# Optimization experiments

Measured on AMD Instinct MI355X. Metric: run time of the kernel, lower is better.

## Reference

```python
import jax, jax.numpy as jnp
import numpy as np

TWO_PI = 2.0 * np.pi
LN_EPS = 1e-5


def _gelu(x):
    return jax.nn.gelu(x, approximate=False)


def _layer_norm(h):
    mu = jnp.mean(h, axis=-1, keepdims=True)
    var = jnp.mean(jnp.square(h - mu), axis=-1, keepdims=True)
    return (h - mu) * jax.lax.rsqrt(var + LN_EPS)


def _torsion_field(x, W, b, tf, tc):
    # x: [B, in], W: [out, in], tf: [order, out, in], tc: scalar
    base = x @ W.T + b
    corr = jnp.zeros_like(base)
    order = tf.shape[0]
    for n in range(order):
        lo = x @ tf[n].T  # [B, out]
        phase = TWO_PI * (n + 1) * lo / (jnp.mean(jnp.abs(lo)) + 1e-8)
        corr = corr + jnp.sin(phase) * lo / (n + 1)
    return base + jax.nn.sigmoid(tc) * corr


def setup_inputs() -> dict:
    key = jax.random.key(0)
    ks = jax.random.split(key, 16)
    B, D_IN, D_R, D_I, D_O, D_H = 2097152, 6, 4, 16, 4, 8
    ts = 0.1
    inp = {
        "x": jax.random.normal(ks[0], (B, D_IN), dtype=jnp.float32),
        # input_projection
        "W_in": jax.random.normal(ks[1], (D_R, D_IN), dtype=jnp.float32) * 0.1,
        "b_in": jnp.zeros((D_R,), jnp.float32),
        # layer1_reciprocal (MiniTorsionField, order=2)
        "r_w": jax.random.normal(ks[2], (D_R, D_R), dtype=jnp.float32) * 0.1,
        "r_b": jnp.zeros((D_R,), jnp.float32),
        "r_tf": jax.random.normal(ks[3], (2, D_R, D_R), dtype=jnp.float32) * ts,
        "r_tc": jnp.float32(0.5),
        # layer1_internal (MiniTorsionField, order=3, strength*0.8)
        "i_w": jax.random.normal(ks[4], (D_I, D_I), dtype=jnp.float32) * 0.1,
        "i_b": jnp.zeros((D_I,), jnp.float32),
        "i_tf": jax.random.normal(ks[5], (3, D_I, D_I), dtype=jnp.float32) * (ts * 0.8),
        "i_tc": jnp.float32(0.5),
        # cross flows
        "W_ri": jax.random.normal(ks[6], (D_I, D_R), dtype=jnp.float32) * 0.1,
        "b_ri": jnp.zeros((D_I,), jnp.float32),
        "W_ir": jax.random.normal(ks[7], (D_R, D_I), dtype=jnp.float32) * 0.1,
        "b_ir": jnp.zeros((D_R,), jnp.float32),
        "flow_gate": jnp.float32(0.5),
        "mem": jax.random.normal(ks[8], (1, D_I), dtype=jnp.float32) * 0.01,
        # output projection: Linear(4,8) -> GELU -> Linear(8,4)
        "W_o1": jax.random.normal(ks[9], (D_H, D_R), dtype=jnp.float32) * 0.1,
        "b_o1": jnp.zeros((D_H,), jnp.float32),
        "W_o2": jax.random.normal(ks[10], (D_O, D_H), dtype=jnp.float32) * 0.1,
        "b_o2": jnp.zeros((D_O,), jnp.float32),
    }
    return inp


def reference(x, W_in, b_in, r_w, r_b, r_tf, r_tc, i_w, i_b, i_tf, i_tc,
              W_ri, b_ri, W_ir, b_ir, flow_gate, mem, W_o1, b_o1, W_o2, b_o2):
    B = x.shape[0]
    x_recip = _gelu(x @ W_in.T + b_in)                      # [B, 4]
    x_internal = jnp.broadcast_to(mem, (B, mem.shape[1]))   # [B, 16]

    h_r = _gelu(_layer_norm(_torsion_field(x_recip, r_w, r_b, r_tf, r_tc)))
    h_i = _gelu(_layer_norm(_torsion_field(x_internal, i_w, i_b, i_tf, i_tc)))

    gate = jax.nn.sigmoid(flow_gate)
    h_i = h_i + gate * (h_r @ W_ri.T + b_ri)
    h_r = h_r + gate * (h_i @ W_ir.T + b_ir)

    out = _gelu(h_r @ W_o1.T + b_o1) @ W_o2.T + b_o2        # [B, 4]
    return out
```

## Files before the change

kernel.cpp:

```cpp
#include <hip/hip_runtime.h>
#include <math.h>

#define TWO_PI_F 6.2831853071795864769f

__device__ __forceinline__ float gelu_f(float v) {
    const float y  = v * 0.70710678118654752f;
    const float ay = fabsf(y);
    const float t  = __builtin_amdgcn_rcpf(fmaf(0.3275911f, ay, 1.0f));
    const float e  = __builtin_amdgcn_exp2f(-1.4426950408889634f * y * y);
    float p = fmaf(1.061405429f, t, -1.453152027f);
    p = fmaf(p, t, 1.421413741f);
    p = fmaf(p, t, -0.284496736f);
    p = fmaf(p, t, 0.254829592f);
    const float erf_abs = 1.0f - p * t * e;
    const float erf_v   = copysignf(erf_abs, v);
    const float hv = 0.5f * v;
    return fmaf(hv, erf_v, hv);
}

__global__ __launch_bounds__(256) void k_sum(
    const float* __restrict__ x,
    const float* __restrict__ W_in, const float* __restrict__ b_in,
    const float* __restrict__ r_tf, const float* __restrict__ r_tc,
    const float* __restrict__ i_w,  const float* __restrict__ i_b,
    const float* __restrict__ i_tf, const float* __restrict__ i_tc,
    const float* __restrict__ W_ri, const float* __restrict__ b_ri,
    const float* __restrict__ W_ir, const float* __restrict__ b_ir,
    const float* __restrict__ flow_gate, const float* __restrict__ mem,
    float2* __restrict__ partials, float* __restrict__ cst, int B)
{
    const int tid = threadIdx.x;
    __shared__ float s_hc[16];
    __shared__ float s_red[8];

    if (blockIdx.x == 0 && tid < 64) {
        const int j = tid & 15;
        float base = i_b[j];
#pragma unroll
        for (int k = 0; k < 16; ++k) base = fmaf(i_w[j*16 + k], mem[k], base);
        float corr = 0.f;
#pragma unroll
        for (int n = 0; n < 3; ++n) {
            float lo = 0.f;
#pragma unroll
            for (int k = 0; k < 16; ++k) lo = fmaf(i_tf[n*256 + j*16 + k], mem[k], lo);
            float a = fabsf(lo);
            a += __shfl_xor(a, 1); a += __shfl_xor(a, 2); a += __shfl_xor(a, 4); a += __shfl_xor(a, 8);
            const float mean = a * (1.0f/16.0f);
            const float phase = TWO_PI_F * (float)(n+1) * lo / (mean + 1e-8f);
            corr = fmaf(sinf(phase), lo / (float)(n+1), corr);
        }
        const float sc = 1.0f / (1.0f + expf(-i_tc[0]));
        const float t = fmaf(sc, corr, base);
        float mu = t;
        mu += __shfl_xor(mu, 1); mu += __shfl_xor(mu, 2); mu += __shfl_xor(mu, 4); mu += __shfl_xor(mu, 8);
        mu *= (1.0f/16.0f);
        const float d = t - mu;
        float v = d*d;
        v += __shfl_xor(v, 1); v += __shfl_xor(v, 2); v += __shfl_xor(v, 4); v += __shfl_xor(v, 8);
        v *= (1.0f/16.0f);
        const float h = gelu_f(d * rsqrtf(v + 1e-5f));
        if (tid < 16) s_hc[j] = h;
    }
    __syncthreads();
    if (blockIdx.x == 0) {
        const float g = 1.0f / (1.0f + expf(-flow_gate[0]));
        if (tid < 4) {
            float acc = 0.f;
#pragma unroll
            for (int m = 0; m < 16; ++m) acc = fmaf(W_ir[tid*16 + m], fmaf(g, b_ri[m], s_hc[m]), acc);
            cst[24 + tid] = g * (acc + b_ir[tid]);
        }
        if (tid < 16) {
            const int l = tid >> 2, j = tid & 3;
            float M = 0.f;
#pragma unroll
            for (int m = 0; m < 16; ++m) M = fmaf(W_ir[l*16 + m], W_ri[m*4 + j], M);
            cst[8 + tid] = g * g * M;
        }
        if (tid == 0) cst[2] = 1.0f / (1.0f + expf(-r_tc[0]));
    }

    const int npairs = B >> 1;
    const int TT = gridDim.x * blockDim.x;
    const int gtid = blockIdx.x * blockDim.x + tid;
    float s0 = 0.f, s1 = 0.f;
    for (int p = gtid; p < npairs; p += TT) {
        const float4* xp = (const float4*)(x + (size_t)p * 12);
        float4 q0 = xp[0], q1 = xp[1], q2 = xp[2];
        float xv[2][6] = {{q0.x, q0.y, q0.z, q0.w, q1.x, q1.y},
                          {q1.z, q1.w, q2.x, q2.y, q2.z, q2.w}};
#pragma unroll
        for (int r = 0; r < 2; ++r) {
            float xr[4];
#pragma unroll
            for (int j = 0; j < 4; ++j) {
                float a = b_in[j];
#pragma unroll
                for (int k = 0; k < 6; ++k) a = fmaf(W_in[j*6+k], xv[r][k], a);
                xr[j] = gelu_f(a);
            }
#pragma unroll
            for (int j = 0; j < 4; ++j) {
                float l0 = 0.f, l1 = 0.f;
#pragma unroll
                for (int k = 0; k < 4; ++k) {
                    l0 = fmaf(r_tf[j*4+k],      xr[k], l0);
                    l1 = fmaf(r_tf[16 + j*4+k], xr[k], l1);
                }
                s0 += fabsf(l0);
                s1 += fabsf(l1);
            }
        }
    }
    if ((B & 1) && gtid == 0) {
        const float* xs = x + (size_t)(B-1) * 6;
        float xr[4];
#pragma unroll
        for (int j = 0; j < 4; ++j) {
            float a = b_in[j];
#pragma unroll
            for (int k = 0; k < 6; ++k) a = fmaf(W_in[j*6+k], xs[k], a);
            xr[j] = gelu_f(a);
        }
#pragma unroll
        for (int j = 0; j < 4; ++j) {
            float l0 = 0.f, l1 = 0.f;
#pragma unroll
            for (int k = 0; k < 4; ++k) {
                l0 = fmaf(r_tf[j*4+k],      xr[k], l0);
                l1 = fmaf(r_tf[16 + j*4+k], xr[k], l1);
            }
            s0 += fabsf(l0);
            s1 += fabsf(l1);
        }
    }
#pragma unroll
    for (int off = 32; off > 0; off >>= 1) {
        s0 += __shfl_down(s0, off);
        s1 += __shfl_down(s1, off);
    }
    if ((tid & 63) == 0) { s_red[(tid>>6)*2] = s0; s_red[(tid>>6)*2+1] = s1; }
    __syncthreads();
    if (tid == 0) {
        partials[blockIdx.x] = make_float2(s_red[0]+s_red[2]+s_red[4]+s_red[6],
                                           s_red[1]+s_red[3]+s_red[5]+s_red[7]);
    }
}

__global__ __launch_bounds__(256) void k_main(
    const float* __restrict__ x,
    const float* __restrict__ W_in, const float* __restrict__ b_in,
    const float* __restrict__ r_w,  const float* __restrict__ r_b,
    const float* __restrict__ r_tf,
    const float* __restrict__ W_o1, const float* __restrict__ b_o1,
    const float* __restrict__ W_o2, const float* __restrict__ b_o2,
    const float2* __restrict__ partials, int nb,
    const float* __restrict__ cst,
    float* __restrict__ out, int B)
{
    const int tid = threadIdx.x;
    __shared__ float s_red[8];
    __shared__ float s_c[2];

    float t0 = 0.f, t1 = 0.f;
    for (int k = tid; k < nb; k += 256) {
        const float2 pr = partials[k];
        t0 += pr.x; t1 += pr.y;
    }
#pragma unroll
    for (int off = 32; off > 0; off >>= 1) {
        t0 += __shfl_down(t0, off);
        t1 += __shfl_down(t1, off);
    }
    if ((tid & 63) == 0) { s_red[(tid>>6)*2] = t0; s_red[(tid>>6)*2+1] = t1; }
    __syncthreads();
    if (tid == 0) {
        const float u0 = s_red[0]+s_red[2]+s_red[4]+s_red[6];
        const float u1 = s_red[1]+s_red[3]+s_red[5]+s_red[7];
        const float m0 = u0 / (4.0f * (float)B);
        const float m1 = u1 / (4.0f * (float)B);
        s_c[0] = TWO_PI_F * 1.0f / (m0 + 1e-8f);
        s_c[1] = TWO_PI_F * 2.0f / (m1 + 1e-8f);
    }
    __syncthreads();
    const float c0 = s_c[0], c1 = s_c[1];
    const float sr = cst[2];

    float m4[16], cvec[4];
#pragma unroll
    for (int i = 0; i < 16; ++i) m4[i] = cst[8 + i];
#pragma unroll
    for (int i = 0; i < 4; ++i)  cvec[i] = cst[24 + i];

    const int npairs = B >> 1;
    const int TT = gridDim.x * blockDim.x;
    const int gtid = blockIdx.x * blockDim.x + tid;

    for (int p = gtid; p < npairs; p += TT) {
        const float4* xp = (const float4*)(x + (size_t)p * 12);
        float4 q0 = xp[0], q1 = xp[1], q2 = xp[2];
        float xv[2][6] = {{q0.x, q0.y, q0.z, q0.w, q1.x, q1.y},
                          {q1.z, q1.w, q2.x, q2.y, q2.z, q2.w}};
#pragma unroll
        for (int r = 0; r < 2; ++r) {
            float xr[4];
#pragma unroll
            for (int j = 0; j < 4; ++j) {
                float a = b_in[j];
#pragma unroll
                for (int k = 0; k < 6; ++k) a = fmaf(W_in[j*6+k], xv[r][k], a);
                xr[j] = gelu_f(a);
            }
            float t[4];
#pragma unroll
            for (int j = 0; j < 4; ++j) {
                float l0 = 0.f, l1 = 0.f, bse = r_b[j];
#pragma unroll
                for (int k = 0; k < 4; ++k) {
                    l0  = fmaf(r_tf[j*4+k],      xr[k], l0);
                    l1  = fmaf(r_tf[16 + j*4+k], xr[k], l1);
                    bse = fmaf(r_w[j*4+k],       xr[k], bse);
                }
                const float corr = __sinf(c0 * l0) * l0 + 0.5f * __sinf(c1 * l1) * l1;
                t[j] = fmaf(sr, corr, bse);
            }
            const float mu = 0.25f * (t[0] + t[1] + t[2] + t[3]);
            float d0 = t[0]-mu, d1 = t[1]-mu, d2 = t[2]-mu, d3 = t[3]-mu;
            const float var = 0.25f * (d0*d0 + d1*d1 + d2*d2 + d3*d3);
            const float inv = rsqrtf(var + 1e-5f);
            float hr[4] = { gelu_f(d0*inv), gelu_f(d1*inv), gelu_f(d2*inv), gelu_f(d3*inv) };

            float h2[4];
#pragma unroll
            for (int l = 0; l < 4; ++l) {
                float a = hr[l] + cvec[l];
#pragma unroll
                for (int j = 0; j < 4; ++j) a = fmaf(m4[l*4+j], hr[j], a);
                h2[l] = a;
            }
            float hid[8];
#pragma unroll
            for (int h = 0; h < 8; ++h) {
                float a = b_o1[h];
#pragma unroll
                for (int l = 0; l < 4; ++l) a = fmaf(W_o1[h*4+l], h2[l], a);
                hid[h] = gelu_f(a);
            }
            float o[4];
#pragma unroll
            for (int oo = 0; oo < 4; ++oo) {
                float a = b_o2[oo];
#pragma unroll
                for (int h = 0; h < 8; ++h) a = fmaf(W_o2[oo*8+h], hid[h], a);
                o[oo] = a;
            }
            ((float4*)out)[(size_t)2*p + r] = make_float4(o[0], o[1], o[2], o[3]);
        }
    }

    if ((B & 1) && gtid == 0) {
        const float* xs = x + (size_t)(B-1) * 6;
        float xr[4];
#pragma unroll
        for (int j = 0; j < 4; ++j) {
            float a = b_in[j];
#pragma unroll
            for (int k = 0; k < 6; ++k) a = fmaf(W_in[j*6+k], xs[k], a);
            xr[j] = gelu_f(a);
        }
        float t[4];
#pragma unroll
        for (int j = 0; j < 4; ++j) {
            float l0 = 0.f, l1 = 0.f, bse = r_b[j];
#pragma unroll
            for (int k = 0; k < 4; ++k) {
                l0  = fmaf(r_tf[j*4+k],      xr[k], l0);
                l1  = fmaf(r_tf[16 + j*4+k], xr[k], l1);
                bse = fmaf(r_w[j*4+k],       xr[k], bse);
            }
            const float corr = __sinf(c0 * l0) * l0 + 0.5f * __sinf(c1 * l1) * l1;
            t[j] = fmaf(sr, corr, bse);
        }
        const float mu = 0.25f * (t[0] + t[1] + t[2] + t[3]);
        float d0 = t[0]-mu, d1 = t[1]-mu, d2 = t[2]-mu, d3 = t[3]-mu;
        const float var = 0.25f * (d0*d0 + d1*d1 + d2*d2 + d3*d3);
        const float inv = rsqrtf(var + 1e-5f);
        float hr[4] = { gelu_f(d0*inv), gelu_f(d1*inv), gelu_f(d2*inv), gelu_f(d3*inv) };
        float h2[4];
#pragma unroll
        for (int l = 0; l < 4; ++l) {
            float a = hr[l] + cvec[l];
#pragma unroll
            for (int j = 0; j < 4; ++j) a = fmaf(m4[l*4+j], hr[j], a);
            h2[l] = a;
        }
        float hid[8];
#pragma unroll
        for (int h = 0; h < 8; ++h) {
            float a = b_o1[h];
#pragma unroll
            for (int l = 0; l < 4; ++l) a = fmaf(W_o1[h*4+l], h2[l], a);
            hid[h] = gelu_f(a);
        }
        float o[4];
#pragma unroll
        for (int oo = 0; oo < 4; ++oo) {
            float a = b_o2[oo];
#pragma unroll
            for (int h = 0; h < 8; ++h) a = fmaf(W_o2[oo*8+h], hid[h], a);
            o[oo] = a;
        }
        ((float4*)out)[(size_t)B - 1] = make_float4(o[0], o[1], o[2], o[3]);
    }
}

extern "C" void kernel_launch(void* const* d_in, const int* in_sizes, int n_in,
                              void* d_out, int out_size, void* d_ws, size_t ws_size,
                              hipStream_t stream)
{
    const float* x    = (const float*)d_in[0];
    const float* W_in = (const float*)d_in[1];
    const float* b_in = (const float*)d_in[2];
    const float* r_w  = (const float*)d_in[3];
    const float* r_b  = (const float*)d_in[4];
    const float* r_tf = (const float*)d_in[5];
    const float* r_tc = (const float*)d_in[6];
    const float* i_w  = (const float*)d_in[7];
    const float* i_b  = (const float*)d_in[8];
    const float* i_tf = (const float*)d_in[9];
    const float* i_tc = (const float*)d_in[10];
    const float* W_ri = (const float*)d_in[11];
    const float* b_ri = (const float*)d_in[12];
    const float* W_ir = (const float*)d_in[13];
    const float* b_ir = (const float*)d_in[14];
    const float* fg   = (const float*)d_in[15];
    const float* mem  = (const float*)d_in[16];
    const float* W_o1 = (const float*)d_in[17];
    const float* b_o1 = (const float*)d_in[18];
    const float* W_o2 = (const float*)d_in[19];
    const float* b_o2 = (const float*)d_in[20];
    float* out = (float*)d_out;
    float* ws  = (float*)d_ws;

    const int B = in_sizes[0] / 6;

    int NB1 = 1024;
    const long cap = (long)(ws_size / 4) - 64;
    if (cap < 2L * NB1) NB1 = (int)(cap / 2);
    if (NB1 < 1) NB1 = 1;
    float*  cst      = ws;
    float2* partials = (float2*)(ws + 64);

    k_sum<<<NB1, 256, 0, stream>>>(x, W_in, b_in, r_tf, r_tc, i_w, i_b, i_tf, i_tc,
                                   W_ri, b_ri, W_ir, b_ir, fg, mem, partials, cst, B);

    int NB2 = 2048;
    const int npairs = B >> 1;
    if (NB2 * 256 > npairs + 255) NB2 = (npairs + 255) / 256;
    if (NB2 < 1) NB2 = 1;
    k_main<<<NB2, 256, 0, stream>>>(x, W_in, b_in, r_w, r_b, r_tf,
                                    W_o1, b_o1, W_o2, b_o2,
                                    partials, NB1, cst, out, B);
}
```

Baseline: 53.05 us.

## Pack two rows into float2 math, fold constants, and use cheaper GELU and sin

Both kernels now process the two rows of each pair together using float2 vector types and element-wise FMA, which can map to packed FP32 instructions. Weights are folded ahead of time: sigmoid and 2π factors go into the torsion weights, and the cross-flow matrix and offset are merged into the first output layer, computed once in block 0. GELU uses a shorter erf polynomial, sin uses the hardware revolution-based instruction, and outputs are written with nontemporal stores. Grid size and launch bounds also change; the lower-order erf approximation adds some numerical error.

```diff
diff --git a/kernel.cpp b/kernel.cpp
--- a/kernel.cpp
+++ b/kernel.cpp
@@ -3,22 +3,58 @@
 
 #define TWO_PI_F 6.2831853071795864769f
 
-__device__ __forceinline__ float gelu_f(float v) {
+typedef float v2f __attribute__((ext_vector_type(2)));
+typedef float v4f __attribute__((ext_vector_type(4)));
+
+static __device__ __forceinline__ v2f v2s(float s) { return (v2f){s, s}; }
+
+static __device__ __forceinline__ v2f fma2(v2f a, v2f b, v2f c) {
+#if __has_builtin(__builtin_elementwise_fma)
+    return __builtin_elementwise_fma(a, b, c);
+#else
+    return (v2f){ fmaf(a.x, b.x, c.x), fmaf(a.y, b.y, c.y) };
+#endif
+}
+
+static __device__ __forceinline__ float sin_rev(float x) {
+#if __has_builtin(__builtin_amdgcn_sinf)
+    return __builtin_amdgcn_sinf(x);
+#else
+    return __sinf(TWO_PI_F * x);
+#endif
+}
+
+static __device__ __forceinline__ float gelu_s(float v) {
     const float y  = v * 0.70710678118654752f;
     const float ay = fabsf(y);
-    const float t  = __builtin_amdgcn_rcpf(fmaf(0.3275911f, ay, 1.0f));
-    const float e  = __builtin_amdgcn_exp2f(-1.4426950408889634f * y * y);
-    float p = fmaf(1.061405429f, t, -1.453152027f);
-    p = fmaf(p, t, 1.421413741f);
-    p = fmaf(p, t, -0.284496736f);
-    p = fmaf(p, t, 0.254829592f);
+    const float t  = __builtin_amdgcn_rcpf(fmaf(0.47047f, ay, 1.0f));
+    const float e  = __builtin_amdgcn_exp2f(y * y * -1.4426950408889634f);
+    float p = fmaf(0.7478556f, t, -0.0958798f);
+    p = fmaf(p, t, 0.3480242f);
     const float erf_abs = 1.0f - p * t * e;
-    const float erf_v   = copysignf(erf_abs, v);
+    const float erf_v   = __builtin_copysignf(erf_abs, v);
     const float hv = 0.5f * v;
     return fmaf(hv, erf_v, hv);
 }
 
-__global__ __launch_bounds__(256) void k_sum(
+static __device__ __forceinline__ v2f gelu2(v2f v) {
+    v2f y  = v * 0.70710678118654752f;
+    v2f ay = (v2f){ fabsf(y.x), fabsf(y.y) };
+    v2f td = fma2(v2s(0.47047f), ay, v2s(1.0f));
+    v2f t  = (v2f){ __builtin_amdgcn_rcpf(td.x), __builtin_amdgcn_rcpf(td.y) };
+    v2f yy = y * y;
+    v2f e  = (v2f){ __builtin_amdgcn_exp2f(yy.x * -1.4426950408889634f),
+                    __builtin_amdgcn_exp2f(yy.y * -1.4426950408889634f) };
+    v2f p  = fma2(v2s(0.7478556f), t, v2s(-0.0958798f));
+    p = fma2(p, t, v2s(0.3480242f));
+    v2f erfabs = v2s(1.0f) - (p * t) * e;
+    v2f erf = (v2f){ __builtin_copysignf(erfabs.x, v.x),
+                     __builtin_copysignf(erfabs.y, v.y) };
+    v2f hv = v * 0.5f;
+    return fma2(hv, erf, hv);
+}
+
+__global__ __launch_bounds__(256, 8) void k_sum(
     const float* __restrict__ x,
     const float* __restrict__ W_in, const float* __restrict__ b_in,
     const float* __restrict__ r_tf, const float* __restrict__ r_tc,
@@ -27,92 +63,112 @@
     const float* __restrict__ W_ri, const float* __restrict__ b_ri,
     const float* __restrict__ W_ir, const float* __restrict__ b_ir,
     const float* __restrict__ flow_gate, const float* __restrict__ mem,
+    const float* __restrict__ W_o1, const float* __restrict__ b_o1,
     float2* __restrict__ partials, float* __restrict__ cst, int B)
 {
     const int tid = threadIdx.x;
-    __shared__ float s_hc[16];
-    __shared__ float s_red[8];
-
-    if (blockIdx.x == 0 && tid < 64) {
-        const int j = tid & 15;
-        float base = i_b[j];
-#pragma unroll
-        for (int k = 0; k < 16; ++k) base = fmaf(i_w[j*16 + k], mem[k], base);
-        float corr = 0.f;
-#pragma unroll
-        for (int n = 0; n < 3; ++n) {
-            float lo = 0.f;
-#pragma unroll
-            for (int k = 0; k < 16; ++k) lo = fmaf(i_tf[n*256 + j*16 + k], mem[k], lo);
-            float a = fabsf(lo);
-            a += __shfl_xor(a, 1); a += __shfl_xor(a, 2); a += __shfl_xor(a, 4); a += __shfl_xor(a, 8);
-            const float mean = a * (1.0f/16.0f);
-            const float phase = TWO_PI_F * (float)(n+1) * lo / (mean + 1e-8f);
-            corr = fmaf(sinf(phase), lo / (float)(n+1), corr);
-        }
-        const float sc = 1.0f / (1.0f + expf(-i_tc[0]));
-        const float t = fmaf(sc, corr, base);
-        float mu = t;
-        mu += __shfl_xor(mu, 1); mu += __shfl_xor(mu, 2); mu += __shfl_xor(mu, 4); mu += __shfl_xor(mu, 8);
-        mu *= (1.0f/16.0f);
-        const float d = t - mu;
-        float v = d*d;
-        v += __shfl_xor(v, 1); v += __shfl_xor(v, 2); v += __shfl_xor(v, 4); v += __shfl_xor(v, 8);
-        v *= (1.0f/16.0f);
-        const float h = gelu_f(d * rsqrtf(v + 1e-5f));
-        if (tid < 16) s_hc[j] = h;
-    }
-    __syncthreads();
+    __shared__ float s_hc[16], s_cv[4], s_m4[16], s_red[8];
+
     if (blockIdx.x == 0) {
-        const float g = 1.0f / (1.0f + expf(-flow_gate[0]));
+        if (tid < 64) {
+            const int j = tid & 15;
+            float base = i_b[j];
+#pragma unroll
+            for (int k = 0; k < 16; ++k) base = fmaf(i_w[j*16 + k], mem[k], base);
+            float corr = 0.f;
+#pragma unroll
+            for (int n = 0; n < 3; ++n) {
+                float lo = 0.f;
+#pragma unroll
+                for (int k = 0; k < 16; ++k) lo = fmaf(i_tf[n*256 + j*16 + k], mem[k], lo);
+                float a = fabsf(lo);
+                a += __shfl_xor(a, 1); a += __shfl_xor(a, 2);
+                a += __shfl_xor(a, 4); a += __shfl_xor(a, 8);
+                const float mean = a * (1.0f/16.0f);
+                const float phase = TWO_PI_F * (float)(n+1) * lo / (mean + 1e-8f);
+                corr = fmaf(sinf(phase), lo / (float)(n+1), corr);
+            }
+            const float sc = 1.0f / (1.0f + expf(-i_tc[0]));
+            const float t = fmaf(sc, corr, base);
+            float mu = t;
+            mu += __shfl_xor(mu, 1); mu += __shfl_xor(mu, 2);
+            mu += __shfl_xor(mu, 4); mu += __shfl_xor(mu, 8);
+            mu *= (1.0f/16.0f);
+            const float d = t - mu;
+            float v = d*d;
+            v += __shfl_xor(v, 1); v += __shfl_xor(v, 2);
+            v += __shfl_xor(v, 4); v += __shfl_xor(v, 8);
+            v *= (1.0f/16.0f);
+            const float h = gelu_s(d * rsqrtf(v + 1e-5f));
+            if (tid < 16) s_hc[j] = h;
+        }
+        __syncthreads();
+        const float g  = 1.0f / (1.0f + expf(-flow_gate[0]));
+        const float sr = 1.0f / (1.0f + expf(-r_tc[0]));
         if (tid < 4) {
             float acc = 0.f;
 #pragma unroll
-            for (int m = 0; m < 16; ++m) acc = fmaf(W_ir[tid*16 + m], fmaf(g, b_ri[m], s_hc[m]), acc);
-            cst[24 + tid] = g * (acc + b_ir[tid]);
+            for (int m = 0; m < 16; ++m)
+                acc = fmaf(W_ir[tid*16 + m], fmaf(g, b_ri[m], s_hc[m]), acc);
+            s_cv[tid] = g * (acc + b_ir[tid]);
         }
         if (tid < 16) {
             const int l = tid >> 2, j = tid & 3;
             float M = 0.f;
 #pragma unroll
             for (int m = 0; m < 16; ++m) M = fmaf(W_ir[l*16 + m], W_ri[m*4 + j], M);
-            cst[8 + tid] = g * g * M;
-        }
-        if (tid == 0) cst[2] = 1.0f / (1.0f + expf(-r_tc[0]));
+            s_m4[tid] = g * g * M;
+            cst[8  + tid] = sr * r_tf[tid];
+            cst[24 + tid] = 0.5f * sr * r_tf[16 + tid];
+        }
+        if (tid == 0) cst[0] = sr;
+        __syncthreads();
+        if (tid < 32) {
+            const int h = tid >> 2, j = tid & 3;
+            float we = 0.f;
+#pragma unroll
+            for (int l = 0; l < 4; ++l)
+                we = fmaf(W_o1[h*4 + l], ((l == j) ? 1.0f : 0.0f) + s_m4[l*4 + j], we);
+            cst[40 + tid] = we;
+        }
+        if (tid < 8) {
+            float be = b_o1[tid];
+#pragma unroll
+            for (int l = 0; l < 4; ++l) be = fmaf(W_o1[tid*4 + l], s_cv[l], be);
+            cst[72 + tid] = be;
+        }
     }
 
     const int npairs = B >> 1;
     const int TT = gridDim.x * blockDim.x;
     const int gtid = blockIdx.x * blockDim.x + tid;
-    float s0 = 0.f, s1 = 0.f;
+    v2f a0 = v2s(0.f), a1 = v2s(0.f);
     for (int p = gtid; p < npairs; p += TT) {
         const float4* xp = (const float4*)(x + (size_t)p * 12);
         float4 q0 = xp[0], q1 = xp[1], q2 = xp[2];
-        float xv[2][6] = {{q0.x, q0.y, q0.z, q0.w, q1.x, q1.y},
-                          {q1.z, q1.w, q2.x, q2.y, q2.z, q2.w}};
-#pragma unroll
-        for (int r = 0; r < 2; ++r) {
-            float xr[4];
-#pragma unroll
-            for (int j = 0; j < 4; ++j) {
-                float a = b_in[j];
-#pragma unroll
-                for (int k = 0; k < 6; ++k) a = fmaf(W_in[j*6+k], xv[r][k], a);
-                xr[j] = gelu_f(a);
+        v2f xv[6] = { {q0.x, q1.z}, {q0.y, q1.w}, {q0.z, q2.x},
+                      {q0.w, q2.y}, {q1.x, q2.z}, {q1.y, q2.w} };
+        v2f xr[4];
+#pragma unroll
+        for (int j = 0; j < 4; ++j) {
+            v2f a = v2s(b_in[j]);
+#pragma unroll
+            for (int k = 0; k < 6; ++k) a = fma2(v2s(W_in[j*6+k]), xv[k], a);
+            xr[j] = gelu2(a);
+        }
+#pragma unroll
+        for (int j = 0; j < 4; ++j) {
+            v2f l0 = v2s(0.f), l1 = v2s(0.f);
+#pragma unroll
+            for (int k = 0; k < 4; ++k) {
+                l0 = fma2(v2s(r_tf[j*4+k]),      xr[k], l0);
+                l1 = fma2(v2s(r_tf[16 + j*4+k]), xr[k], l1);
             }
-#pragma unroll
-            for (int j = 0; j < 4; ++j) {
-                float l0 = 0.f, l1 = 0.f;
-#pragma unroll
-                for (int k = 0; k < 4; ++k) {
-                    l0 = fmaf(r_tf[j*4+k],      xr[k], l0);
-                    l1 = fmaf(r_tf[16 + j*4+k], xr[k], l1);
-                }
-                s0 += fabsf(l0);
-                s1 += fabsf(l1);
-            }
-        }
-    }
+            a0 += (v2f){ fabsf(l0.x), fabsf(l0.y) };
+            a1 += (v2f){ fabsf(l1.x), fabsf(l1.y) };
+        }
+    }
+    float s0 = a0.x + a0.y, s1 = a1.x + a1.y;
     if ((B & 1) && gtid == 0) {
         const float* xs = x + (size_t)(B-1) * 6;
         float xr[4];
@@ -121,7 +177,7 @@
             float a = b_in[j];
 #pragma unroll
             for (int k = 0; k < 6; ++k) a = fmaf(W_in[j*6+k], xs[k], a);
-            xr[j] = gelu_f(a);
+            xr[j] = gelu_s(a);
         }
 #pragma unroll
         for (int j = 0; j < 4; ++j) {
@@ -148,12 +204,10 @@
     }
 }
 
-__global__ __launch_bounds__(256) void k_main(
+__global__ __launch_bounds__(256, 4) void k_main(
     const float* __restrict__ x,
     const float* __restrict__ W_in, const float* __restrict__ b_in,
     const float* __restrict__ r_w,  const float* __restrict__ r_b,
-    const float* __restrict__ r_tf,
-    const float* __restrict__ W_o1, const float* __restrict__ b_o1,
     const float* __restrict__ W_o2, const float* __restrict__ b_o2,
     const float2* __restrict__ partials, int nb,
     const float* __restrict__ cst,
@@ -175,23 +229,17 @@
     }
     if ((tid & 63) == 0) { s_red[(tid>>6)*2] = t0; s_red[(tid>>6)*2+1] = t1; }
     __syncthreads();
+    const float sr = cst[0];
     if (tid == 0) {
         const float u0 = s_red[0]+s_red[2]+s_red[4]+s_red[6];
         const float u1 = s_red[1]+s_red[3]+s_red[5]+s_red[7];
         const float m0 = u0 / (4.0f * (float)B);
         const float m1 = u1 / (4.0f * (float)B);
-        s_c[0] = TWO_PI_F * 1.0f / (m0 + 1e-8f);
-        s_c[1] = TWO_PI_F * 2.0f / (m1 + 1e-8f);
+        s_c[0] = 1.0f / ((m0 + 1e-8f) * sr);
+        s_c[1] = 4.0f / ((m1 + 1e-8f) * sr);
     }
     __syncthreads();
-    const float c0 = s_c[0], c1 = s_c[1];
-    const float sr = cst[2];
-
-    float m4[16], cvec[4];
-#pragma unroll
-    for (int i = 0; i < 16; ++i) m4[i] = cst[8 + i];
-#pragma unroll
-    for (int i = 0; i < 4; ++i)  cvec[i] = cst[24 + i];
+    const float C0 = s_c[0], C1 = s_c[1];
 
     const int npairs = B >> 1;
     const int TT = gridDim.x * blockDim.x;
@@ -200,63 +248,63 @@
     for (int p = gtid; p < npairs; p += TT) {
         const float4* xp = (const float4*)(x + (size_t)p * 12);
         float4 q0 = xp[0], q1 = xp[1], q2 = xp[2];
-        float xv[2][6] = {{q0.x, q0.y, q0.z, q0.w, q1.x, q1.y},
-                          {q1.z, q1.w, q2.x, q2.y, q2.z, q2.w}};
-#pragma unroll
-        for (int r = 0; r < 2; ++r) {
-            float xr[4];
-#pragma unroll
-            for (int j = 0; j < 4; ++j) {
-                float a = b_in[j];
-#pragma unroll
-                for (int k = 0; k < 6; ++k) a = fmaf(W_in[j*6+k], xv[r][k], a);
-                xr[j] = gelu_f(a);
+        v2f xv[6] = { {q0.x, q1.z}, {q0.y, q1.w}, {q0.z, q2.x},
+                      {q0.w, q2.y}, {q1.x, q2.z}, {q1.y, q2.w} };
+
+        v2f xr[4];
+#pragma unroll
+        for (int j = 0; j < 4; ++j) {
+            v2f a = v2s(b_in[j]);
+#pragma unroll
+            for (int k = 0; k < 6; ++k) a = fma2(v2s(W_in[j*6+k]), xv[k], a);
+            xr[j] = gelu2(a);
+        }
+
+        v2f t[4];
+#pragma unroll
+        for (int j = 0; j < 4; ++j) {
+            v2f L0 = v2s(0.f), L1 = v2s(0.f), bse = v2s(r_b[j]);
+#pragma unroll
+            for (int k = 0; k < 4; ++k) {
+                L0  = fma2(v2s(cst[8  + j*4+k]), xr[k], L0);
+                L1  = fma2(v2s(cst[24 + j*4+k]), xr[k], L1);
+                bse = fma2(v2s(r_w[j*4+k]),      xr[k], bse);
             }
-            float t[4];
-#pragma unroll
-            for (int j = 0; j < 4; ++j) {
-                float l0 = 0.f, l1 = 0.f, bse = r_b[j];
-#pragma unroll
-                for (int k = 0; k < 4; ++k) {
-                    l0  = fmaf(r_tf[j*4+k],      xr[k], l0);
-                    l1  = fmaf(r_tf[16 + j*4+k], xr[k], l1);
-                    bse = fmaf(r_w[j*4+k],       xr[k], bse);
-                }
-                const float corr = __sinf(c0 * l0) * l0 + 0.5f * __sinf(c1 * l1) * l1;
-                t[j] = fmaf(sr, corr, bse);
-            }
-            const float mu = 0.25f * (t[0] + t[1] + t[2] + t[3]);
-            float d0 = t[0]-mu, d1 = t[1]-mu, d2 = t[2]-mu, d3 = t[3]-mu;
-            const float var = 0.25f * (d0*d0 + d1*d1 + d2*d2 + d3*d3);
-            const float inv = rsqrtf(var + 1e-5f);
-            float hr[4] = { gelu_f(d0*inv), gelu_f(d1*inv), gelu_f(d2*inv), gelu_f(d3*inv) };
-
-            float h2[4];
-#pragma unroll
-            for (int l = 0; l < 4; ++l) {
-                float a = hr[l] + cvec[l];
-#pragma unroll
-                for (int j = 0; j < 4; ++j) a = fmaf(m4[l*4+j], hr[j], a);
-                h2[l] = a;
-            }
-            float hid[8];
-#pragma unroll
-            for (int h = 0; h < 8; ++h) {
-                float a = b_o1[h];
-#pragma unroll
-                for (int l = 0; l < 4; ++l) a = fmaf(W_o1[h*4+l], h2[l], a);
-                hid[h] = gelu_f(a);
-            }
-            float o[4];
-#pragma unroll
-            for (int oo = 0; oo < 4; ++oo) {
-                float a = b_o2[oo];
-#pragma unroll
-                for (int h = 0; h < 8; ++h) a = fmaf(W_o2[oo*8+h], hid[h], a);
-                o[oo] = a;
-            }
-            ((float4*)out)[(size_t)2*p + r] = make_float4(o[0], o[1], o[2], o[3]);
-        }
+            v2f sa = (v2f){ sin_rev(C0 * L0.x), sin_rev(C0 * L0.y) };
+            v2f sb = (v2f){ sin_rev(C1 * L1.x), sin_rev(C1 * L1.y) };
+            t[j] = fma2(sa, L0, fma2(sb, L1, bse));
+        }
+
+        const v2f mu = (t[0] + t[1] + t[2] + t[3]) * 0.25f;
+        v2f d0 = t[0]-mu, d1 = t[1]-mu, d2 = t[2]-mu, d3 = t[3]-mu;
+        v2f var = d0*d0;
+        var = fma2(d1, d1, var);
+        var = fma2(d2, d2, var);
+        var = fma2(d3, d3, var);
+        var = var * 0.25f + 1e-5f;
+        const v2f inv = (v2f){ __builtin_amdgcn_rsqf(var.x), __builtin_amdgcn_rsqf(var.y) };
+        v2f hr[4] = { gelu2(d0*inv), gelu2(d1*inv), gelu2(d2*inv), gelu2(d3*inv) };
+
+        v2f hid[8];
+#pragma unroll
+        for (int h = 0; h < 8; ++h) {
+            v2f a = v2s(cst[72 + h]);
+#pragma unroll
+            for (int j = 0; j < 4; ++j) a = fma2(v2s(cst[40 + h*4+j]), hr[j], a);
+            hid[h] = gelu2(a);
+        }
+        v2f o[4];
+#pragma unroll
+        for (int oo = 0; oo < 4; ++oo) {
+            v2f a = v2s(b_o2[oo]);
+#pragma unroll
+            for (int h = 0; h < 8; ++h) a = fma2(v2s(W_o2[oo*8+h]), hid[h], a);
+            o[oo] = a;
+        }
+        v4f r0 = (v4f){ o[0].x, o[1].x, o[2].x, o[3].x };
+        v4f r1 = (v4f){ o[0].y, o[1].y, o[2].y, o[3].y };
+        __builtin_nontemporal_store(r0, (v4f*)out + (size_t)2*p);
+        __builtin_nontemporal_store(r1, (v4f*)out + (size_t)2*p + 1);
     }
 
     if ((B & 1) && gtid == 0) {
@@ -267,41 +315,32 @@
             float a = b_in[j];
 #pragma unroll
             for (int k = 0; k < 6; ++k) a = fmaf(W_in[j*6+k], xs[k], a);
-            xr[j] = gelu_f(a);
+            xr[j] = gelu_s(a);
         }
         float t[4];
 #pragma unroll
         for (int j = 0; j < 4; ++j) {
-            float l0 = 0.f, l1 = 0.f, bse = r_b[j];
+            float L0 = 0.f, L1 = 0.f, bse = r_b[j];
 #pragma unroll
             for (int k = 0; k < 4; ++k) {
-                l0  = fmaf(r_tf[j*4+k],      xr[k], l0);
-                l1  = fmaf(r_tf[16 + j*4+k], xr[k], l1);
-                bse = fmaf(r_w[j*4+k],       xr[k], bse);
+                L0  = fmaf(cst[8  + j*4+k], xr[k], L0);
+                L1  = fmaf(cst[24 + j*4+k], xr[k], L1);
+                bse = fmaf(r_w[j*4+k],      xr[k], bse);
             }
-            const float corr = __sinf(c0 * l0) * l0 + 0.5f * __sinf(c1 * l1) * l1;
-            t[j] = fmaf(sr, corr, bse);
-        }
-        const float mu = 0.25f * (t[0] + t[1] + t[2] + t[3]);
-        float d0 = t[0]-mu, d1 = t[1]-mu, d2 = t[2]-mu, d3 = t[3]-mu;
+            t[j] = fmaf(sin_rev(C0*L0), L0, fmaf(sin_rev(C1*L1), L1, bse));
+        }
+        const float mu = 0.25f * (t[0]+t[1]+t[2]+t[3]);
+        float d0=t[0]-mu, d1=t[1]-mu, d2=t[2]-mu, d3=t[3]-mu;
         const float var = 0.25f * (d0*d0 + d1*d1 + d2*d2 + d3*d3);
-        const float inv = rsqrtf(var + 1e-5f);
-        float hr[4] = { gelu_f(d0*inv), gelu_f(d1*inv), gelu_f(d2*inv), gelu_f(d3*inv) };
-        float h2[4];
-#pragma unroll
-        for (int l = 0; l < 4; ++l) {
-            float a = hr[l] + cvec[l];
-#pragma unroll
-            for (int j = 0; j < 4; ++j) a = fmaf(m4[l*4+j], hr[j], a);
-            h2[l] = a;
-        }
+        const float inv = __builtin_amdgcn_rsqf(var + 1e-5f);
+        float hr[4] = { gelu_s(d0*inv), gelu_s(d1*inv), gelu_s(d2*inv), gelu_s(d3*inv) };
         float hid[8];
 #pragma unroll
         for (int h = 0; h < 8; ++h) {
-            float a = b_o1[h];
-#pragma unroll
-            for (int l = 0; l < 4; ++l) a = fmaf(W_o1[h*4+l], h2[l], a);
-            hid[h] = gelu_f(a);
+            float a = cst[72 + h];
+#pragma unroll
+            for (int j = 0; j < 4; ++j) a = fmaf(cst[40 + h*4+j], hr[j], a);
+            hid[h] = gelu_s(a);
         }
         float o[4];
 #pragma unroll
@@ -344,22 +383,22 @@
     float* ws  = (float*)d_ws;
 
     const int B = in_sizes[0] / 6;
+    const int npairs = B >> 1;
 
     int NB1 = 1024;
-    const long cap = (long)(ws_size / 4) - 64;
+    const long cap = (long)(ws_size / 4) - 128;
     if (cap < 2L * NB1) NB1 = (int)(cap / 2);
     if (NB1 < 1) NB1 = 1;
     float*  cst      = ws;
-    float2* partials = (float2*)(ws + 64);
+    float2* partials = (float2*)(ws + 128);
 
     k_sum<<<NB1, 256, 0, stream>>>(x, W_in, b_in, r_tf, r_tc, i_w, i_b, i_tf, i_tc,
-                                   W_ri, b_ri, W_ir, b_ir, fg, mem, partials, cst, B);
-
-    int NB2 = 2048;
-    const int npairs = B >> 1;
-    if (NB2 * 256 > npairs + 255) NB2 = (npairs + 255) / 256;
+                                   W_ri, b_ri, W_ir, b_ir, fg, mem, W_o1, b_o1,
+                                   partials, cst, B);
+
+    int NB2 = (npairs + 511) / 512;
     if (NB2 < 1) NB2 = 1;
-    k_main<<<NB2, 256, 0, stream>>>(x, W_in, b_in, r_w, r_b, r_tf,
-                                    W_o1, b_o1, W_o2, b_o2,
+    if (NB2 > 8192) NB2 = 8192;
+    k_main<<<NB2, 256, 0, stream>>>(x, W_in, b_in, r_w, r_b, W_o2, b_o2,
                                     partials, NB1, cst, out, B);
 }
```

Measured after the change: 49.53 us. 6.6% less time.

## Replace GELU with shared-memory LUT, fold cross-flow into W_o1, add constants kernel

Applied to the files above, without the earlier changes.

Replaces the erf-based GELU with a 2048-entry linearly interpolated CDF lookup table, built in shared memory by every block of both streaming kernels. Adds a single-block middle kernel that reduces the partial sums and precomputes the folded constants: sigmoid-scaled torsion weights, phase scales in revolutions for the hardware sin, and W_o1 combined with the cross-flow matrix and bias. The main kernel therefore skips the h2 matmul and the per-block partial reduction, and writes its output with nontemporal stores. In exchange it adds an extra launch and a per-block LUT build, and the table clamps inputs to [-6, 6] and approximates GELU with interpolation error.

```diff
diff --git a/kernel.cpp b/kernel.cpp
--- a/kernel.cpp
+++ b/kernel.cpp
@@ -2,89 +2,68 @@
 #include <math.h>
 
 #define TWO_PI_F 6.2831853071795864769f
-
-__device__ __forceinline__ float gelu_f(float v) {
+#define LUT_N    2048
+#define LUT_SCALE 170.66666667f
+#define LUT_STEP  0.005859375f
+
+static __device__ __forceinline__ float sin_rev(float x) {
+#if __has_builtin(__builtin_amdgcn_sinf)
+    return __builtin_amdgcn_sinf(x);
+#else
+    return __sinf(TWO_PI_F * x);
+#endif
+}
+
+static __device__ __forceinline__ float cdf_acc(float v) {
     const float y  = v * 0.70710678118654752f;
     const float ay = fabsf(y);
     const float t  = __builtin_amdgcn_rcpf(fmaf(0.3275911f, ay, 1.0f));
-    const float e  = __builtin_amdgcn_exp2f(-1.4426950408889634f * y * y);
+    const float e  = __builtin_amdgcn_exp2f(y * y * -1.4426950408889634f);
     float p = fmaf(1.061405429f, t, -1.453152027f);
     p = fmaf(p, t, 1.421413741f);
     p = fmaf(p, t, -0.284496736f);
     p = fmaf(p, t, 0.254829592f);
     const float erf_abs = 1.0f - p * t * e;
-    const float erf_v   = copysignf(erf_abs, v);
-    const float hv = 0.5f * v;
-    return fmaf(hv, erf_v, hv);
-}
-
-__global__ __launch_bounds__(256) void k_sum(
+    const float erf_v   = __builtin_copysignf(erf_abs, v);
+    return fmaf(0.5f, erf_v, 0.5f);
+}
+
+static __device__ __forceinline__ float gelu_s(float v) { return v * cdf_acc(v); }
+
+static __device__ __forceinline__ float gelu_lut(float x, const float2* __restrict__ lut) {
+    float f = fminf(fmaxf(fmaf(x, LUT_SCALE, 1024.0f), 0.0f), 2047.5f);
+    float ff = floorf(f);
+    float fr = f - ff;
+    float2 e = lut[(int)ff];
+    return x * fmaf(fr, e.y, e.x);
+}
+
+static __device__ __forceinline__ void build_lut(float2* lut, int tid) {
+    for (int i = tid; i < LUT_N; i += 256) {
+        float x0 = fmaf((float)i, LUT_STEP, -6.0f);
+        float t0 = cdf_acc(x0);
+        float t1 = cdf_acc(x0 + LUT_STEP);
+        lut[i] = make_float2(t0, t1 - t0);
+    }
+}
+
+__global__ __launch_bounds__(256, 8) void k_sum(
     const float* __restrict__ x,
     const float* __restrict__ W_in, const float* __restrict__ b_in,
-    const float* __restrict__ r_tf, const float* __restrict__ r_tc,
-    const float* __restrict__ i_w,  const float* __restrict__ i_b,
-    const float* __restrict__ i_tf, const float* __restrict__ i_tc,
-    const float* __restrict__ W_ri, const float* __restrict__ b_ri,
-    const float* __restrict__ W_ir, const float* __restrict__ b_ir,
-    const float* __restrict__ flow_gate, const float* __restrict__ mem,
-    float2* __restrict__ partials, float* __restrict__ cst, int B)
+    const float* __restrict__ r_tf,
+    float2* __restrict__ partials, int B)
 {
     const int tid = threadIdx.x;
-    __shared__ float s_hc[16];
+    __shared__ float2 s_lut[LUT_N];
     __shared__ float s_red[8];
-
-    if (blockIdx.x == 0 && tid < 64) {
-        const int j = tid & 15;
-        float base = i_b[j];
-#pragma unroll
-        for (int k = 0; k < 16; ++k) base = fmaf(i_w[j*16 + k], mem[k], base);
-        float corr = 0.f;
-#pragma unroll
-        for (int n = 0; n < 3; ++n) {
-            float lo = 0.f;
-#pragma unroll
-            for (int k = 0; k < 16; ++k) lo = fmaf(i_tf[n*256 + j*16 + k], mem[k], lo);
-            float a = fabsf(lo);
-            a += __shfl_xor(a, 1); a += __shfl_xor(a, 2); a += __shfl_xor(a, 4); a += __shfl_xor(a, 8);
-            const float mean = a * (1.0f/16.0f);
-            const float phase = TWO_PI_F * (float)(n+1) * lo / (mean + 1e-8f);
-            corr = fmaf(sinf(phase), lo / (float)(n+1), corr);
-        }
-        const float sc = 1.0f / (1.0f + expf(-i_tc[0]));
-        const float t = fmaf(sc, corr, base);
-        float mu = t;
-        mu += __shfl_xor(mu, 1); mu += __shfl_xor(mu, 2); mu += __shfl_xor(mu, 4); mu += __shfl_xor(mu, 8);
-        mu *= (1.0f/16.0f);
-        const float d = t - mu;
-        float v = d*d;
-        v += __shfl_xor(v, 1); v += __shfl_xor(v, 2); v += __shfl_xor(v, 4); v += __shfl_xor(v, 8);
-        v *= (1.0f/16.0f);
-        const float h = gelu_f(d * rsqrtf(v + 1e-5f));
-        if (tid < 16) s_hc[j] = h;
-    }
-    __syncthreads();
-    if (blockIdx.x == 0) {
-        const float g = 1.0f / (1.0f + expf(-flow_gate[0]));
-        if (tid < 4) {
-            float acc = 0.f;
-#pragma unroll
-            for (int m = 0; m < 16; ++m) acc = fmaf(W_ir[tid*16 + m], fmaf(g, b_ri[m], s_hc[m]), acc);
-            cst[24 + tid] = g * (acc + b_ir[tid]);
-        }
-        if (tid < 16) {
-            const int l = tid >> 2, j = tid & 3;
-            float M = 0.f;
-#pragma unroll
-            for (int m = 0; m < 16; ++m) M = fmaf(W_ir[l*16 + m], W_ri[m*4 + j], M);
-            cst[8 + tid] = g * g * M;
-        }
-        if (tid == 0) cst[2] = 1.0f / (1.0f + expf(-r_tc[0]));
-    }
+    build_lut(s_lut, tid);
+    __syncthreads();
 
     const int npairs = B >> 1;
     const int TT = gridDim.x * blockDim.x;
     const int gtid = blockIdx.x * blockDim.x + tid;
     float s0 = 0.f, s1 = 0.f;
+
     for (int p = gtid; p < npairs; p += TT) {
         const float4* xp = (const float4*)(x + (size_t)p * 12);
         float4 q0 = xp[0], q1 = xp[1], q2 = xp[2];
@@ -98,7 +77,7 @@
                 float a = b_in[j];
 #pragma unroll
                 for (int k = 0; k < 6; ++k) a = fmaf(W_in[j*6+k], xv[r][k], a);
-                xr[j] = gelu_f(a);
+                xr[j] = gelu_lut(a, s_lut);
             }
 #pragma unroll
             for (int j = 0; j < 4; ++j) {
@@ -121,7 +100,7 @@
             float a = b_in[j];
 #pragma unroll
             for (int k = 0; k < 6; ++k) a = fmaf(W_in[j*6+k], xs[k], a);
-            xr[j] = gelu_f(a);
+            xr[j] = gelu_lut(a, s_lut);
         }
 #pragma unroll
         for (int j = 0; j < 4; ++j) {
@@ -148,20 +127,19 @@
     }
 }
 
-__global__ __launch_bounds__(256) void k_main(
-    const float* __restrict__ x,
-    const float* __restrict__ W_in, const float* __restrict__ b_in,
-    const float* __restrict__ r_w,  const float* __restrict__ r_b,
-    const float* __restrict__ r_tf,
+__global__ __launch_bounds__(256) void k_mid(
+    const float2* __restrict__ partials, int nb, int B,
+    const float* __restrict__ i_w,  const float* __restrict__ i_b,
+    const float* __restrict__ i_tf, const float* __restrict__ i_tc,
+    const float* __restrict__ W_ri, const float* __restrict__ b_ri,
+    const float* __restrict__ W_ir, const float* __restrict__ b_ir,
+    const float* __restrict__ flow_gate, const float* __restrict__ mem,
     const float* __restrict__ W_o1, const float* __restrict__ b_o1,
-    const float* __restrict__ W_o2, const float* __restrict__ b_o2,
-    const float2* __restrict__ partials, int nb,
-    const float* __restrict__ cst,
-    float* __restrict__ out, int B)
+    const float* __restrict__ r_tf, const float* __restrict__ r_tc,
+    float* __restrict__ cst)
 {
     const int tid = threadIdx.x;
-    __shared__ float s_red[8];
-    __shared__ float s_c[2];
+    __shared__ float s_red[8], s_hc[16], s_cv[4], s_m4[16];
 
     float t0 = 0.f, t1 = 0.f;
     for (int k = tid; k < nb; k += 256) {
@@ -175,23 +153,97 @@
     }
     if ((tid & 63) == 0) { s_red[(tid>>6)*2] = t0; s_red[(tid>>6)*2+1] = t1; }
     __syncthreads();
+    const float sr = 1.0f / (1.0f + expf(-r_tc[0]));
     if (tid == 0) {
         const float u0 = s_red[0]+s_red[2]+s_red[4]+s_red[6];
         const float u1 = s_red[1]+s_red[3]+s_red[5]+s_red[7];
         const float m0 = u0 / (4.0f * (float)B);
         const float m1 = u1 / (4.0f * (float)B);
-        s_c[0] = TWO_PI_F * 1.0f / (m0 + 1e-8f);
-        s_c[1] = TWO_PI_F * 2.0f / (m1 + 1e-8f);
-    }
-    __syncthreads();
-    const float c0 = s_c[0], c1 = s_c[1];
-    const float sr = cst[2];
-
-    float m4[16], cvec[4];
-#pragma unroll
-    for (int i = 0; i < 16; ++i) m4[i] = cst[8 + i];
-#pragma unroll
-    for (int i = 0; i < 4; ++i)  cvec[i] = cst[24 + i];
+        cst[0] = 1.0f / ((m0 + 1e-8f) * sr);
+        cst[1] = 4.0f / ((m1 + 1e-8f) * sr);
+    }
+
+    if (tid < 64) {
+        const int j = tid & 15;
+        float base = i_b[j];
+#pragma unroll
+        for (int k = 0; k < 16; ++k) base = fmaf(i_w[j*16 + k], mem[k], base);
+        float corr = 0.f;
+#pragma unroll
+        for (int n = 0; n < 3; ++n) {
+            float lo = 0.f;
+#pragma unroll
+            for (int k = 0; k < 16; ++k) lo = fmaf(i_tf[n*256 + j*16 + k], mem[k], lo);
+            float a = fabsf(lo);
+            a += __shfl_xor(a, 1); a += __shfl_xor(a, 2);
+            a += __shfl_xor(a, 4); a += __shfl_xor(a, 8);
+            const float mean = a * (1.0f/16.0f);
+            const float phase = TWO_PI_F * (float)(n+1) * lo / (mean + 1e-8f);
+            corr = fmaf(sinf(phase), lo / (float)(n+1), corr);
+        }
+        const float sc = 1.0f / (1.0f + expf(-i_tc[0]));
+        const float t = fmaf(sc, corr, base);
+        float mu = t;
+        mu += __shfl_xor(mu, 1); mu += __shfl_xor(mu, 2);
+        mu += __shfl_xor(mu, 4); mu += __shfl_xor(mu, 8);
+        mu *= (1.0f/16.0f);
+        const float d = t - mu;
+        float v = d*d;
+        v += __shfl_xor(v, 1); v += __shfl_xor(v, 2);
+        v += __shfl_xor(v, 4); v += __shfl_xor(v, 8);
+        v *= (1.0f/16.0f);
+        const float h = gelu_s(d * rsqrtf(v + 1e-5f));
+        if (tid < 16) s_hc[j] = h;
+    }
+    __syncthreads();
+    const float g = 1.0f / (1.0f + expf(-flow_gate[0]));
+    if (tid < 4) {
+        float acc = 0.f;
+#pragma unroll
+        for (int m = 0; m < 16; ++m)
+            acc = fmaf(W_ir[tid*16 + m], fmaf(g, b_ri[m], s_hc[m]), acc);
+        s_cv[tid] = g * (acc + b_ir[tid]);
+    }
+    if (tid < 16) {
+        const int l = tid >> 2, j = tid & 3;
+        float M = 0.f;
+#pragma unroll
+        for (int m = 0; m < 16; ++m) M = fmaf(W_ir[l*16 + m], W_ri[m*4 + j], M);
+        s_m4[tid] = g * g * M;
+        cst[8  + tid] = sr * r_tf[tid];
+        cst[24 + tid] = 0.5f * sr * r_tf[16 + tid];
+    }
+    __syncthreads();
+    if (tid < 32) {
+        const int h = tid >> 2, j = tid & 3;
+        float we = 0.f;
+#pragma unroll
+        for (int l = 0; l < 4; ++l)
+            we = fmaf(W_o1[h*4 + l], ((l == j) ? 1.0f : 0.0f) + s_m4[l*4 + j], we);
+        cst[40 + tid] = we;
+    }
+    if (tid < 8) {
+        float be = b_o1[tid];
+#pragma unroll
+        for (int l = 0; l < 4; ++l) be = fmaf(W_o1[tid*4 + l], s_cv[l], be);
+        cst[72 + tid] = be;
+    }
+}
+
+__global__ __launch_bounds__(256, 4) void k_main(
+    const float* __restrict__ x,
+    const float* __restrict__ W_in, const float* __restrict__ b_in,
+    const float* __restrict__ r_w,  const float* __restrict__ r_b,
+    const float* __restrict__ W_o2, const float* __restrict__ b_o2,
+    const float* __restrict__ cst,
+    float* __restrict__ out, int B)
+{
+    const int tid = threadIdx.x;
+    __shared__ float2 s_lut[LUT_N];
+    build_lut(s_lut, tid);
+    __syncthreads();
+
+    const float C0 = cst[0], C1 = cst[1];
 
     const int npairs = B >> 1;
     const int TT = gridDim.x * blockDim.x;
@@ -210,42 +262,34 @@
                 float a = b_in[j];
 #pragma unroll
                 for (int k = 0; k < 6; ++k) a = fmaf(W_in[j*6+k], xv[r][k], a);
-                xr[j] = gelu_f(a);
+                xr[j] = gelu_lut(a, s_lut);
             }
             float t[4];
 #pragma unroll
             for (int j = 0; j < 4; ++j) {
-                float l0 = 0.f, l1 = 0.f, bse = r_b[j];
+                float L0 = 0.f, L1 = 0.f, bse = r_b[j];
 #pragma unroll
                 for (int k = 0; k < 4; ++k) {
-                    l0  = fmaf(r_tf[j*4+k],      xr[k], l0);
-                    l1  = fmaf(r_tf[16 + j*4+k], xr[k], l1);
-                    bse = fmaf(r_w[j*4+k],       xr[k], bse);
+                    L0  = fmaf(cst[8  + j*4+k], xr[k], L0);
+                    L1  = fmaf(cst[24 + j*4+k], xr[k], L1);
+                    bse = fmaf(r_w[j*4+k],      xr[k], bse);
                 }
-                const float corr = __sinf(c0 * l0) * l0 + 0.5f * __sinf(c1 * l1) * l1;
-                t[j] = fmaf(sr, corr, bse);
+                t[j] = fmaf(sin_rev(C0*L0), L0, fmaf(sin_rev(C1*L1), L1, bse));
             }
             const float mu = 0.25f * (t[0] + t[1] + t[2] + t[3]);
             float d0 = t[0]-mu, d1 = t[1]-mu, d2 = t[2]-mu, d3 = t[3]-mu;
-            const float var = 0.25f * (d0*d0 + d1*d1 + d2*d2 + d3*d3);
-            const float inv = rsqrtf(var + 1e-5f);
-            float hr[4] = { gelu_f(d0*inv), gelu_f(d1*inv), gelu_f(d2*inv), gelu_f(d3*inv) };
-
-            float h2[4];
-#pragma unroll
-            for (int l = 0; l < 4; ++l) {
-                float a = hr[l] + cvec[l];
-#pragma unroll
-                for (int j = 0; j < 4; ++j) a = fmaf(m4[l*4+j], hr[j], a);
-                h2[l] = a;
-            }
+            float var = fmaf(d0, d0, fmaf(d1, d1, fmaf(d2, d2, d3*d3)));
+            const float inv = __builtin_amdgcn_rsqf(fmaf(0.25f, var, 1e-5f));
+            float hr[4] = { gelu_lut(d0*inv, s_lut), gelu_lut(d1*inv, s_lut),
+                            gelu_lut(d2*inv, s_lut), gelu_lut(d3*inv, s_lut) };
+
             float hid[8];
 #pragma unroll
             for (int h = 0; h < 8; ++h) {
-                float a = b_o1[h];
-#pragma unroll
-                for (int l = 0; l < 4; ++l) a = fmaf(W_o1[h*4+l], h2[l], a);
-                hid[h] = gelu_f(a);
+                float a = cst[72 + h];
+#pragma unroll
+                for (int j = 0; j < 4; ++j) a = fmaf(cst[40 + h*4+j], hr[j], a);
+                hid[h] = gelu_lut(a, s_lut);
             }
             float o[4];
 #pragma unroll
@@ -255,7 +299,11 @@
                 for (int h = 0; h < 8; ++h) a = fmaf(W_o2[oo*8+h], hid[h], a);
                 o[oo] = a;
             }
-            ((float4*)out)[(size_t)2*p + r] = make_float4(o[0], o[1], o[2], o[3]);
+            float* op = out + (size_t)8*p + (size_t)4*r;
+            __builtin_nontemporal_store(o[0], op + 0);
+            __builtin_nontemporal_store(o[1], op + 1);
+            __builtin_nontemporal_store(o[2], op + 2);
+            __builtin_nontemporal_store(o[3], op + 3);
         }
     }
 
@@ -267,41 +315,33 @@
             float a = b_in[j];
 #pragma unroll
             for (int k = 0; k < 6; ++k) a = fmaf(W_in[j*6+k], xs[k], a);
-            xr[j] = gelu_f(a);
+            xr[j] = gelu_lut(a, s_lut);
         }
         float t[4];
 #pragma unroll
         for (int j = 0; j < 4; ++j) {
-            float l0 = 0.f, l1 = 0.f, bse = r_b[j];
+            float L0 = 0.f, L1 = 0.f, bse = r_b[j];
 #pragma unroll
             for (int k = 0; k < 4; ++k) {
-                l0  = fmaf(r_tf[j*4+k],      xr[k], l0);
-                l1  = fmaf(r_tf[16 + j*4+k], xr[k], l1);
-                bse = fmaf(r_w[j*4+k],       xr[k], bse);
-            }
-            const float corr = __sinf(c0 * l0) * l0 + 0.5f * __sinf(c1 * l1) * l1;
-            t[j] = fmaf(sr, corr, bse);
-        }
-        const float mu = 0.25f * (t[0] + t[1] + t[2] + t[3]);
-        float d0 = t[0]-mu, d1 = t[1]-mu, d2 = t[2]-mu, d3 = t[3]-mu;
+                L0  = fmaf(cst[8  + j*4+k], xr[k], L0);
+                L1  = fmaf(cst[24 + j*4+k], xr[k], L1);
+                bse = fmaf(r_w[j*4+k],      xr[k], bse);
+            }
+            t[j] = fmaf(sin_rev(C0*L0), L0, fmaf(sin_rev(C1*L1), L1, bse));
+        }
+        const float mu = 0.25f * (t[0]+t[1]+t[2]+t[3]);
+        float d0=t[0]-mu, d1=t[1]-mu, d2=t[2]-mu, d3=t[3]-mu;
         const float var = 0.25f * (d0*d0 + d1*d1 + d2*d2 + d3*d3);
-        const float inv = rsqrtf(var + 1e-5f);
-        float hr[4] = { gelu_f(d0*inv), gelu_f(d1*inv), gelu_f(d2*inv), gelu_f(d3*inv) };
-        float h2[4];
-#pragma unroll
-        for (int l = 0; l < 4; ++l) {
-            float a = hr[l] + cvec[l];
-#pragma unroll
-            for (int j = 0; j < 4; ++j) a = fmaf(m4[l*4+j], hr[j], a);
-            h2[l] = a;
-        }
+        const float inv = __builtin_amdgcn_rsqf(var + 1e-5f);
+        float hr[4] = { gelu_lut(d0*inv, s_lut), gelu_lut(d1*inv, s_lut),
+                        gelu_lut(d2*inv, s_lut), gelu_lut(d3*inv, s_lut) };
         float hid[8];
 #pragma unroll
         for (int h = 0; h < 8; ++h) {
-            float a = b_o1[h];
-#pragma unroll
-            for (int l = 0; l < 4; ++l) a = fmaf(W_o1[h*4+l], h2[l], a);
-            hid[h] = gelu_f(a);
+            float a = cst[72 + h];
+#pragma unroll
+            for (int j = 0; j < 4; ++j) a = fmaf(cst[40 + h*4+j], hr[j], a);
+            hid[h] = gelu_lut(a, s_lut);
         }
         float o[4];
 #pragma unroll
@@ -346,20 +386,22 @@
     const int B = in_sizes[0] / 6;
 
     int NB1 = 1024;
-    const long cap = (long)(ws_size / 4) - 64;
+    const long cap = (long)(ws_size / 4) - 128;
     if (cap < 2L * NB1) NB1 = (int)(cap / 2);
     if (NB1 < 1) NB1 = 1;
     float*  cst      = ws;
-    float2* partials = (float2*)(ws + 64);
-
-    k_sum<<<NB1, 256, 0, stream>>>(x, W_in, b_in, r_tf, r_tc, i_w, i_b, i_tf, i_tc,
-                                   W_ri, b_ri, W_ir, b_ir, fg, mem, partials, cst, B);
+    float2* partials = (float2*)(ws + 128);
+
+    k_sum<<<NB1, 256, 0, stream>>>(x, W_in, b_in, r_tf, partials, B);
+
+    k_mid<<<1, 256, 0, stream>>>(partials, NB1, B, i_w, i_b, i_tf, i_tc,
+                                 W_ri, b_ri, W_ir, b_ir, fg, mem, W_o1, b_o1,
+                                 r_tf, r_tc, cst);
 
     int NB2 = 2048;
     const int npairs = B >> 1;
     if (NB2 * 256 > npairs + 255) NB2 = (npairs + 255) / 256;
     if (NB2 < 1) NB2 = 1;
-    k_main<<<NB2, 256, 0, stream>>>(x, W_in, b_in, r_w, r_b, r_tf,
-                                    W_o1, b_o1, W_o2, b_o2,
-                                    partials, NB1, cst, out, B);
-}
+    k_main<<<NB2, 256, 0, stream>>>(x, W_in, b_in, r_w, r_b, W_o2, b_o2,
+                                    cst, out, B);
+}
```

Result: faster. 46.90 us (-11.6%).
